# Kernel optimization log

Measured on AMD Instinct MI355X. Metric: run time of the kernel, lower is better.

The kernel has to match this reference:

```python
import jax, jax.numpy as jnp
import numpy as np


def setup_inputs() -> dict:
    key = jax.random.key(0)
    k = jax.random.split(key, 5)
    B, S, D, H = 4, 2048, 2048, 8192
    scale1 = 1.0 / np.sqrt(D)
    scale2 = 1.0 / np.sqrt(H)
    return {
        "x": jax.random.normal(k[0], (B, S, D), dtype=jnp.float32),
        "w1": jax.random.normal(k[1], (H, D), dtype=jnp.float32) * scale1,
        "b1": jax.random.normal(k[2], (H,), dtype=jnp.float32) * scale1,
        "w2": jax.random.normal(k[3], (D, H), dtype=jnp.float32) * scale2,
        "b2": jax.random.normal(k[4], (D,), dtype=jnp.float32) * scale2,
    }


def reference(x, w1, b1, w2, b2):
    # fc1: [B,S,D] @ [D,H] -> [B,S,H]
    h = jnp.einsum("bsd,hd->bsh", x, w1) + b1
    # squared ReLU activation
    a = jnp.square(jax.nn.relu(h))
    # fc2: [B,S,H] @ [H,D] -> [B,S,D]
    return jnp.einsum("bsh,dh->bsd", a, w2) + b2
```

## Files before the change

kernel.cpp:

```cpp
#include <hip/hip_runtime.h>
#include <hip/hip_bf16.h>
#include <stdint.h>

typedef __bf16 bf16x8 __attribute__((ext_vector_type(8)));
typedef float f32x4 __attribute__((ext_vector_type(4)));


__device__ inline void gload_lds16(const void* g, void* lds) {
  __builtin_amdgcn_global_load_lds(
      (const __attribute__((address_space(1))) uint32_t*)(uintptr_t)g,
      (__attribute__((address_space(3))) uint32_t*)(uintptr_t)lds,
      16, 0, 0);
}

__device__ inline short f2bf(float f) {
  union { float f; uint32_t u; } x; x.f = f;
  uint32_t u = x.u;
  u += 0x7fffu + ((u >> 16) & 1u);
  return (short)(u >> 16);
}


__global__ __launch_bounds__(256) void cvt_f32_bf16(
    const float* __restrict__ in, short* __restrict__ out, int n4) {
  int i = blockIdx.x * 256 + threadIdx.x;
  if (i < n4) {
    float4 v = reinterpret_cast<const float4*>(in)[i];
    short4 o;
    o.x = f2bf(v.x); o.y = f2bf(v.y); o.z = f2bf(v.z); o.w = f2bf(v.w);
    reinterpret_cast<short4*>(out)[i] = o;
  }
}


template <int EPI>
__global__ __launch_bounds__(512, 2) void gemm_bt(
    const short* __restrict__ A, const short* __restrict__ B,
    const float* __restrict__ bias, void* __restrict__ Cout,
    int M, int N, int K) {
  __shared__ __align__(16) short lds[4][2][256 * 32];

  const int tid  = threadIdx.x;
  const int wave = tid >> 6;
  const int lane = tid & 63;
  const int wr = wave >> 2;
  const int wc = wave & 3;

  const int nwg = gridDim.x;
  const int w = (blockIdx.x & 7) * (nwg >> 3) + (blockIdx.x >> 3);
  const int gy = M >> 8;
  const int brow = w % gy;
  const int bcol = w / gy;

  f32x4 acc[8][4];
#pragma unroll
  for (int m = 0; m < 8; ++m)
#pragma unroll
    for (int n = 0; n < 4; ++n)
      acc[m][n] = (f32x4){0.f, 0.f, 0.f, 0.f};

  const int nk = K >> 5;

  const int fr = lane & 15, kq = lane >> 4;

  int offA[8], offB[4];
#pragma unroll
  for (int m = 0; m < 8; ++m) {
    int row = wr * 128 + m * 16 + fr;
    int g = row * 4 + kq;
    offA[m] = (g ^ ((g >> 3) & 7)) * 8;
  }
#pragma unroll
  for (int n = 0; n < 4; ++n) {
    int row = wc * 64 + n * 16 + fr;
    int g = row * 4 + kq;
    offB[n] = (g ^ ((g >> 3) & 7)) * 8;
  }

  const int iA0 = tid, iA1 = 512 + tid;
  const int glA0 = iA0 ^ ((iA0 >> 3) & 7), glA1 = iA1 ^ ((iA1 >> 3) & 7);
  const short* pA0 = A + (size_t)(brow * 256 + (glA0 >> 2)) * K + (glA0 & 3) * 8;
  const short* pA1 = A + (size_t)(brow * 256 + (glA1 >> 2)) * K + (glA1 & 3) * 8;
  const short* pB0 = B + (size_t)(bcol * 256 + (glA0 >> 2)) * K + (glA0 & 3) * 8;
  const short* pB1 = B + (size_t)(bcol * 256 + (glA1 >> 2)) * K + (glA1 & 3) * 8;

  auto stageA = [&](int slot) {
    short* base = &lds[slot][0][0];
    gload_lds16(pA0, base + (wave * 64) * 8);
    gload_lds16(pA1, base + (512 + wave * 64) * 8);
    pA0 += 32; pA1 += 32;
  };
  auto stageB = [&](int slot) {
    short* base = &lds[slot][1][0];
    gload_lds16(pB0, base + (wave * 64) * 8);
    gload_lds16(pB1, base + (512 + wave * 64) * 8);
    pB0 += 32; pB1 += 32;
  };

  stageA(0); stageB(0);
  stageA(1); stageB(1);
  stageA(2); stageB(2);
  asm volatile("s_waitcnt vmcnt(8)" ::: "memory");
  __builtin_amdgcn_s_barrier();
  asm volatile("" ::: "memory");

  for (int c = 0; c < nk; ++c) {
    const int slot = c & 3;
    const int sl3 = (c + 3) & 3;
    const bool do_stage = (c + 3) < nk;
    const short* sA = &lds[slot][0][0];
    const short* sB = &lds[slot][1][0];

    if (do_stage) stageA(sl3);
    bf16x8 a[8];
#pragma unroll
    for (int m = 0; m < 8; ++m)
      a[m] = *(const bf16x8*)(sA + offA[m]);
    bf16x8 b0 = *(const bf16x8*)(sB + offB[0]);
    bf16x8 b1 = *(const bf16x8*)(sB + offB[1]);
    __builtin_amdgcn_s_setprio(1);
#pragma unroll
    for (int m = 0; m < 8; ++m) {
      acc[m][0] = __builtin_amdgcn_mfma_f32_16x16x32_bf16(a[m], b0, acc[m][0], 0, 0, 0);
      acc[m][1] = __builtin_amdgcn_mfma_f32_16x16x32_bf16(a[m], b1, acc[m][1], 0, 0, 0);
    }
    __builtin_amdgcn_s_setprio(0);

    if (do_stage) stageB(sl3);
    bf16x8 b2 = *(const bf16x8*)(sB + offB[2]);
    bf16x8 b3 = *(const bf16x8*)(sB + offB[3]);
    __builtin_amdgcn_s_setprio(1);
#pragma unroll
    for (int m = 0; m < 8; ++m) {
      acc[m][2] = __builtin_amdgcn_mfma_f32_16x16x32_bf16(a[m], b2, acc[m][2], 0, 0, 0);
      acc[m][3] = __builtin_amdgcn_mfma_f32_16x16x32_bf16(a[m], b3, acc[m][3], 0, 0, 0);
    }
    __builtin_amdgcn_s_setprio(0);

    if (c < nk - 1) {
      const int rem = nk - 2 - c;
      if (rem >= 2)      asm volatile("s_waitcnt vmcnt(8)" ::: "memory");
      else if (rem == 1) asm volatile("s_waitcnt vmcnt(4)" ::: "memory");
      else               asm volatile("s_waitcnt vmcnt(0)" ::: "memory");
      __builtin_amdgcn_s_barrier();
      asm volatile("" ::: "memory");
    }
  }

  const int q = lane >> 4;
  if (EPI == 0) {
    short* C = (short*)Cout;
#pragma unroll
    for (int m = 0; m < 8; ++m) {
      const int row0 = brow * 256 + wr * 128 + m * 16 + q * 4;
#pragma unroll
      for (int n = 0; n < 4; ++n) {
        const int col = bcol * 256 + wc * 64 + n * 16 + fr;
        const float bv = bias[col];
#pragma unroll
        for (int j = 0; j < 4; ++j) {
          float v = acc[m][n][j] + bv;
          v = v > 0.f ? v * v : 0.f;
          C[(size_t)(row0 + j) * N + col] = f2bf(v);
        }
      }
    }
  } else {
    float* C = (float*)Cout;
#pragma unroll
    for (int m = 0; m < 8; ++m) {
      const int row0 = brow * 256 + wr * 128 + m * 16 + q * 4;
#pragma unroll
      for (int n = 0; n < 4; ++n) {
        const int col = bcol * 256 + wc * 64 + n * 16 + fr;
        const float bv = bias[col];
#pragma unroll
        for (int j = 0; j < 4; ++j)
          C[(size_t)(row0 + j) * N + col] = acc[m][n][j] + bv;
      }
    }
  }
}


extern "C" void kernel_launch(void* const* d_in, const int* in_sizes, int n_in,
                              void* d_out, int out_size, void* d_ws,
                              size_t ws_size, hipStream_t stream) {
  const float* x  = (const float*)d_in[0];
  const float* w1 = (const float*)d_in[1];
  const float* b1 = (const float*)d_in[2];
  const float* w2 = (const float*)d_in[3];
  const float* b2 = (const float*)d_in[4];
  float* out = (float*)d_out;

  const int H = in_sizes[2];
  const int D = in_sizes[4];
  const int M = in_sizes[0] / D;

  short* xb  = (short*)d_ws;
  short* w1b = xb  + (size_t)M * D;
  short* w2b = w1b + (size_t)H * D;
  short* act = w2b + (size_t)D * H;

  {
    int n4 = (M * D) / 4;
    cvt_f32_bf16<<<(n4 + 255) / 256, 256, 0, stream>>>(x, xb, n4);
    n4 = (H * D) / 4;
    cvt_f32_bf16<<<(n4 + 255) / 256, 256, 0, stream>>>(w1, w1b, n4);
    n4 = (D * H) / 4;
    cvt_f32_bf16<<<(n4 + 255) / 256, 256, 0, stream>>>(w2, w2b, n4);
  }

  gemm_bt<0><<<(M / 256) * (H / 256), 512, 0, stream>>>(
      xb, w1b, b1, (void*)act, M, H, D);
  gemm_bt<1><<<(M / 256) * (D / 256), 512, 0, stream>>>(
      act, w2b, b2, (void*)out, M, D, H);
}
```

Measured before the change: 635.9 us.

## Restructure GEMM mainloop into BK=64 double-buffered quadrant ping-pong schedule

```diff
diff --git a/kernel.cpp b/kernel.cpp
--- a/kernel.cpp
+++ b/kernel.cpp
@@ -19,6 +19,10 @@
   u += 0x7fffu + ((u >> 16) & 1u);
   return (short)(u >> 16);
 }
+
+#define BAR() do { asm volatile("" ::: "memory"); \
+                   __builtin_amdgcn_s_barrier();  \
+                   asm volatile("" ::: "memory"); } while (0)
 
 
 __global__ __launch_bounds__(256) void cvt_f32_bf16(
@@ -38,13 +42,14 @@
     const short* __restrict__ A, const short* __restrict__ B,
     const float* __restrict__ bias, void* __restrict__ Cout,
     int M, int N, int K) {
-  __shared__ __align__(16) short lds[4][2][256 * 32];
+  __shared__ __align__(16) short lds[2][4][128 * 64];
 
   const int tid  = threadIdx.x;
   const int wave = tid >> 6;
   const int lane = tid & 63;
   const int wr = wave >> 2;
   const int wc = wave & 3;
+  const int fr = lane & 15, kq = lane >> 4;
 
   const int nwg = gridDim.x;
   const int w = (blockIdx.x & 7) * (nwg >> 3) + (blockIdx.x >> 3);
@@ -59,91 +64,157 @@
     for (int n = 0; n < 4; ++n)
       acc[m][n] = (f32x4){0.f, 0.f, 0.f, 0.f};
 
-  const int nk = K >> 5;
-
-  const int fr = lane & 15, kq = lane >> 4;
-
-  int offA[8], offB[4];
-#pragma unroll
-  for (int m = 0; m < 8; ++m) {
-    int row = wr * 128 + m * 16 + fr;
-    int g = row * 4 + kq;
-    offA[m] = (g ^ ((g >> 3) & 7)) * 8;
-  }
-#pragma unroll
-  for (int n = 0; n < 4; ++n) {
-    int row = wc * 64 + n * 16 + fr;
-    int g = row * 4 + kq;
-    offB[n] = (g ^ ((g >> 3) & 7)) * 8;
-  }
-
-  const int iA0 = tid, iA1 = 512 + tid;
-  const int glA0 = iA0 ^ ((iA0 >> 3) & 7), glA1 = iA1 ^ ((iA1 >> 3) & 7);
-  const short* pA0 = A + (size_t)(brow * 256 + (glA0 >> 2)) * K + (glA0 & 3) * 8;
-  const short* pA1 = A + (size_t)(brow * 256 + (glA1 >> 2)) * K + (glA1 & 3) * 8;
-  const short* pB0 = B + (size_t)(bcol * 256 + (glA0 >> 2)) * K + (glA0 & 3) * 8;
-  const short* pB1 = B + (size_t)(bcol * 256 + (glA1 >> 2)) * K + (glA1 & 3) * 8;
-
-  auto stageA = [&](int slot) {
-    short* base = &lds[slot][0][0];
-    gload_lds16(pA0, base + (wave * 64) * 8);
-    gload_lds16(pA1, base + (512 + wave * 64) * 8);
-    pA0 += 32; pA1 += 32;
-  };
-  auto stageB = [&](int slot) {
-    short* base = &lds[slot][1][0];
-    gload_lds16(pB0, base + (wave * 64) * 8);
-    gload_lds16(pB1, base + (512 + wave * 64) * 8);
-    pB0 += 32; pB1 += 32;
-  };
-
-  stageA(0); stageB(0);
-  stageA(1); stageB(1);
-  stageA(2); stageB(2);
-  asm volatile("s_waitcnt vmcnt(8)" ::: "memory");
-  __builtin_amdgcn_s_barrier();
-  asm volatile("" ::: "memory");
-
-  for (int c = 0; c < nk; ++c) {
-    const int slot = c & 3;
-    const int sl3 = (c + 3) & 3;
-    const bool do_stage = (c + 3) < nk;
-    const short* sA = &lds[slot][0][0];
-    const short* sB = &lds[slot][1][0];
-
-    if (do_stage) stageA(sl3);
-    bf16x8 a[8];
-#pragma unroll
-    for (int m = 0; m < 8; ++m)
-      a[m] = *(const bf16x8*)(sA + offA[m]);
-    bf16x8 b0 = *(const bf16x8*)(sB + offB[0]);
-    bf16x8 b1 = *(const bf16x8*)(sB + offB[1]);
-    __builtin_amdgcn_s_setprio(1);
-#pragma unroll
-    for (int m = 0; m < 8; ++m) {
-      acc[m][0] = __builtin_amdgcn_mfma_f32_16x16x32_bf16(a[m], b0, acc[m][0], 0, 0, 0);
-      acc[m][1] = __builtin_amdgcn_mfma_f32_16x16x32_bf16(a[m], b1, acc[m][1], 0, 0, 0);
-    }
-    __builtin_amdgcn_s_setprio(0);
-
-    if (do_stage) stageB(sl3);
-    bf16x8 b2 = *(const bf16x8*)(sB + offB[2]);
-    bf16x8 b3 = *(const bf16x8*)(sB + offB[3]);
-    __builtin_amdgcn_s_setprio(1);
-#pragma unroll
-    for (int m = 0; m < 8; ++m) {
-      acc[m][2] = __builtin_amdgcn_mfma_f32_16x16x32_bf16(a[m], b2, acc[m][2], 0, 0, 0);
-      acc[m][3] = __builtin_amdgcn_mfma_f32_16x16x32_bf16(a[m], b3, acc[m][3], 0, 0, 0);
-    }
-    __builtin_amdgcn_s_setprio(0);
-
-    if (c < nk - 1) {
-      const int rem = nk - 2 - c;
-      if (rem >= 2)      asm volatile("s_waitcnt vmcnt(8)" ::: "memory");
-      else if (rem == 1) asm volatile("s_waitcnt vmcnt(4)" ::: "memory");
-      else               asm volatile("s_waitcnt vmcnt(0)" ::: "memory");
-      __builtin_amdgcn_s_barrier();
-      asm volatile("" ::: "memory");
+  const int nk = K >> 6;
+
+  int offA[4][2], offB[2][2];
+#pragma unroll
+  for (int m = 0; m < 4; ++m)
+#pragma unroll
+    for (int kk = 0; kk < 2; ++kk) {
+      int r = wr * 64 + m * 16 + fr;
+      int g = r * 8 + kk * 4 + kq;
+      offA[m][kk] = (g ^ (r & 7)) * 16;
+    }
+#pragma unroll
+  for (int n = 0; n < 2; ++n)
+#pragma unroll
+    for (int kk = 0; kk < 2; ++kk) {
+      int r = wc * 32 + n * 16 + fr;
+      int g = r * 8 + kk * 4 + kq;
+      offB[n][kk] = (g ^ (r & 7)) * 16;
+    }
+
+  const int i0 = tid;
+  const int gl0 = i0 ^ ((i0 >> 3) & 7);
+  const int r0 = gl0 >> 3, c0 = gl0 & 7;
+  const size_t rstep = (size_t)128 * K;
+
+  const short* pA[2];
+  const short* pB[2];
+  {
+    const int rb0 = (r0 >> 5) * 64 + (r0 & 31);
+#pragma unroll
+    for (int h = 0; h < 2; ++h) {
+      pA[h] = A + (size_t)(brow * 256 + h * 64 + r0) * K + c0 * 8;
+      pB[h] = B + (size_t)(bcol * 256 + rb0 + h * 32) * K + c0 * 8;
+    }
+  }
+
+  const int dst0 = wave * 512, dst1 = 4096 + wave * 512;
+
+#define STAGE(p, buf, slot)                              \
+  do {                                                   \
+    short* base_ = &lds[buf][slot][0];                   \
+    gload_lds16((p), base_ + dst0);                      \
+    gload_lds16((p) + rstep, base_ + dst1);              \
+    (p) += 64;                                           \
+  } while (0)
+
+  STAGE(pA[0], 0, 0);
+  STAGE(pB[0], 0, 2);
+  STAGE(pB[1], 0, 3);
+  STAGE(pA[1], 0, 1);
+  STAGE(pA[0], 1, 0);
+  STAGE(pB[0], 1, 2);
+  STAGE(pB[1], 1, 3);
+  asm volatile("s_waitcnt vmcnt(6)" ::: "memory");
+  BAR();
+
+  bf16x8 aq[4][2], b0q[2][2], b1q[2][2];
+
+  for (int t = 0; t < nk; ++t) {
+    const int cur = t & 1, nxt = cur ^ 1;
+    const bool s1 = (t + 1) < nk, s2 = (t + 2) < nk;
+
+    if (s1) STAGE(pA[1], nxt, 1);
+    {
+      const char* sA = (const char*)&lds[cur][0][0];
+      const char* sB = (const char*)&lds[cur][2][0];
+#pragma unroll
+      for (int m = 0; m < 4; ++m)
+#pragma unroll
+        for (int kk = 0; kk < 2; ++kk)
+          aq[m][kk] = *(const bf16x8*)(sA + offA[m][kk]);
+#pragma unroll
+      for (int n = 0; n < 2; ++n)
+#pragma unroll
+        for (int kk = 0; kk < 2; ++kk)
+          b0q[n][kk] = *(const bf16x8*)(sB + offB[n][kk]);
+    }
+    BAR();
+    __builtin_amdgcn_s_setprio(1);
+#pragma unroll
+    for (int m = 0; m < 4; ++m)
+#pragma unroll
+      for (int n = 0; n < 2; ++n)
+#pragma unroll
+        for (int kk = 0; kk < 2; ++kk)
+          acc[m][n] = __builtin_amdgcn_mfma_f32_16x16x32_bf16(
+              aq[m][kk], b0q[n][kk], acc[m][n], 0, 0, 0);
+    __builtin_amdgcn_s_setprio(0);
+    BAR();
+
+    if (s2) STAGE(pA[0], cur, 0);
+    {
+      const char* sB = (const char*)&lds[cur][3][0];
+#pragma unroll
+      for (int n = 0; n < 2; ++n)
+#pragma unroll
+        for (int kk = 0; kk < 2; ++kk)
+          b1q[n][kk] = *(const bf16x8*)(sB + offB[n][kk]);
+    }
+    BAR();
+    __builtin_amdgcn_s_setprio(1);
+#pragma unroll
+    for (int m = 0; m < 4; ++m)
+#pragma unroll
+      for (int n = 0; n < 2; ++n)
+#pragma unroll
+        for (int kk = 0; kk < 2; ++kk)
+          acc[m][n + 2] = __builtin_amdgcn_mfma_f32_16x16x32_bf16(
+              aq[m][kk], b1q[n][kk], acc[m][n + 2], 0, 0, 0);
+    __builtin_amdgcn_s_setprio(0);
+    BAR();
+
+    if (s2) STAGE(pB[0], cur, 2);
+    {
+      const char* sA = (const char*)&lds[cur][1][0];
+#pragma unroll
+      for (int m = 0; m < 4; ++m)
+#pragma unroll
+        for (int kk = 0; kk < 2; ++kk)
+          aq[m][kk] = *(const bf16x8*)(sA + offA[m][kk]);
+    }
+    BAR();
+    __builtin_amdgcn_s_setprio(1);
+#pragma unroll
+    for (int m = 0; m < 4; ++m)
+#pragma unroll
+      for (int n = 0; n < 2; ++n)
+#pragma unroll
+        for (int kk = 0; kk < 2; ++kk)
+          acc[m + 4][n + 2] = __builtin_amdgcn_mfma_f32_16x16x32_bf16(
+              aq[m][kk], b1q[n][kk], acc[m + 4][n + 2], 0, 0, 0);
+    __builtin_amdgcn_s_setprio(0);
+    BAR();
+
+    if (s2) STAGE(pB[1], cur, 3);
+    BAR();
+    __builtin_amdgcn_s_setprio(1);
+#pragma unroll
+    for (int m = 0; m < 4; ++m)
+#pragma unroll
+      for (int n = 0; n < 2; ++n)
+#pragma unroll
+        for (int kk = 0; kk < 2; ++kk)
+          acc[m + 4][n] = __builtin_amdgcn_mfma_f32_16x16x32_bf16(
+              aq[m][kk], b0q[n][kk], acc[m + 4][n], 0, 0, 0);
+    __builtin_amdgcn_s_setprio(0);
+
+    if (t < nk - 1) {
+      if (s2) asm volatile("s_waitcnt vmcnt(6)" ::: "memory");
+      else    asm volatile("s_waitcnt vmcnt(0)" ::: "memory");
+      BAR();
     }
   }
 
@@ -180,6 +251,7 @@
       }
     }
   }
+#undef STAGE
 }
 
 
```

Result: faster. 548.8 us (-13.7%).
